# Kernel tuning notes

Hardware: AMD Instinct MI355X
Metric: run time of the kernel (lower is better)

## Reference

```python
import jax, jax.numpy as jnp
import numpy as np

N_IN = 16384
G = 64            # input grid resolution
K_UP = 8          # 2^3 children per voxel for kernel=2 stride=2 generative transpose conv
N_OUT = N_IN * K_UP
G2 = 2 * G        # output grid resolution
NUMS = 32768      # top-k prune budget
C = 64


def _np_coords_and_maps():
    """Build voxel coords, the 27-offset kernel map on upsampled coords, and a fake GT mask."""
    rng = np.random.default_rng(0)
    flat = rng.choice(G ** 3, size=N_IN, replace=False)
    c = np.stack(np.unravel_index(flat, (G, G, G)), axis=1).astype(np.int64)  # [N_IN,3]
    offs2 = np.stack(np.meshgrid(*([[0, 1]] * 3), indexing='ij'), -1).reshape(-1, 3)  # [8,3]
    cu = (2 * c[:, None, :] + offs2[None]).reshape(-1, 3)  # [N_OUT,3], order n*8+k
    lut = np.full(G2 ** 3, N_OUT, dtype=np.int64)
    key = (cu[:, 0] * G2 + cu[:, 1]) * G2 + cu[:, 2]
    lut[key] = np.arange(N_OUT)
    offs3 = np.stack(np.meshgrid(*([[-1, 0, 1]] * 3), indexing='ij'), -1).reshape(-1, 3)  # [27,3]
    nbr = np.empty((27, N_OUT), np.int64)
    for k, d in enumerate(offs3):
        q = cu + d
        valid = ((q >= 0) & (q < G2)).all(1)
        qk = np.where(valid, (q[:, 0] * G2 + q[:, 1]) * G2 + q[:, 2], 0)
        nbr[k] = np.where(valid, lut[qk], N_OUT)  # N_OUT = sentinel 'missing'
    gt = rng.random(N_OUT) < 0.3  # isin(out.C, ground_truth.C) membership mask
    return nbr.astype(np.int32), gt


def setup_inputs() -> dict:
    key = jax.random.key(0)
    ks = jax.random.split(key, 10)
    nbr, gt = _np_coords_and_maps()
    s = 0.05
    rn = lambda k, shape: jax.random.normal(k, shape, jnp.float32) * s
    z = lambda shape: jnp.zeros(shape, jnp.float32)
    return {
        "x_feats": jax.random.normal(ks[0], (N_IN, C), jnp.float32),
        "Wup": rn(ks[1], (K_UP, C, C)), "bup": z((C,)),
        "Wc0": rn(ks[2], (27, C, C)), "bc0": z((C,)),
        "W00": rn(ks[3], (3, 27, C, C // 4)), "b00": z((3, C // 4)),
        "W01": rn(ks[4], (3, 27, C // 4, C // 2)), "b01": z((3, C // 2)),
        "W10": rn(ks[5], (3, C, C // 4)), "b10": z((3, C // 4)),
        "W11": rn(ks[6], (3, 27, C // 4, C // 4)), "b11": z((3, C // 4)),
        "W12": rn(ks[7], (3, C // 4, C // 2)), "b12": z((3, C // 2)),
        "Wcls": rn(ks[8], (27, C, 1)), "bcls": z((1,)),
        "nbr_idx": jnp.asarray(nbr), "mask_true": jnp.asarray(gt),
        "nums": NUMS,
    }


def sparse_conv(feats, nbr, W, b):
    """Gather-GEMM-scatter sparse conv: feats [N,Cin], nbr [K,N] (N = missing), W [K,Cin,Cout]."""
    fp = jnp.concatenate([feats, jnp.zeros((1, feats.shape[1]), feats.dtype)], axis=0)
    def body(acc, wn):
        Wk, nk = wn
        return acc + fp[nk] @ Wk, None
    acc0 = jnp.zeros((feats.shape[0], W.shape[-1]), feats.dtype)
    out, _ = jax.lax.scan(body, acc0, (W, nbr))
    return out + b


def reference(x_feats, Wup, bup, Wc0, bc0, W00, b00, W01, b01, W10, b10, W11, b11, W12, b12, Wcls, bcls, nbr_idx, mask_true, nums):
    # generative transpose conv k=2 s=2: each voxel emits 8 children (no overlaps)
    up = jnp.einsum('nc,kcd->nkd', x_feats, Wup).reshape(-1, Wup.shape[-1]) + bup  # [N_OUT,C]
    out = jax.nn.relu(up)
    out = jax.nn.relu(sparse_conv(out, nbr_idx, Wc0, bc0))
    for i in range(3):  # 3 InceptionResNet blocks
        o0 = sparse_conv(jax.nn.relu(sparse_conv(out, nbr_idx, W00[i], b00[i])), nbr_idx, W01[i], b01[i])
        t = jax.nn.relu(out @ W10[i] + b10[i])            # 1x1 conv
        t = jax.nn.relu(sparse_conv(t, nbr_idx, W11[i], b11[i]))
        o1 = t @ W12[i] + b12[i]                          # 1x1 conv
        out = jnp.concatenate([o0, o1], axis=1) + out
    out_cls = sparse_conv(out, nbr_idx, Wcls, bcls)       # [N_OUT,1]
    _, idx = jax.lax.top_k(out_cls[:, 0], nums)           # istopk
    mask = jnp.zeros((out.shape[0],), bool).at[idx].set(True) | mask_true  # topk + isin(GT)
    pruned = out * mask[:, None].astype(out.dtype)        # pruning as mask (static shape)
    return out_cls, pruned, mask
```

## Files before the change

kernel.cpp:

```cpp
#include <hip/hip_runtime.h>
#include <cstdint>

#define NOUTC 131072
#define NINC  16384
#define CAP   204800
#define NCH   128
#define MAXB  3328

using uint = unsigned int;

__device__ __forceinline__ uint fkey(float v){
  uint u = __float_as_uint(v);
  return (u & 0x80000000u) ? ~u : (u | 0x80000000u);
}

__device__ __forceinline__ int ktap(int o, int q){
  int d0 = ((q>>2)&1) - ((o>>2)&1);
  int d1 = ((q>>1)&1) - ((o>>1)&1);
  int d2 = (q&1) - (o&1);
  return (d0+1)*9 + (d1+1)*3 + (d2+1);
}
__device__ __forceinline__ bool is_sib(int o, int k){
  int k0 = k/9, k1 = (k%9)/3, k2 = k%3;
  int q0 = ((o>>2)&1) + k0 - 1;
  int q1 = ((o>>1)&1) + k1 - 1;
  int q2 = (o&1)      + k2 - 1;
  return (q0>=0 && q0<=1 && q1>=0 && q1<=1 && q2>=0 && q2<=1);
}

__global__ __launch_bounds__(256)
void count_kernel(const int* __restrict__ nbr, uint* __restrict__ counts)
{
  int k = blockIdx.x / NCH, cb = blockIdx.x % NCH;
  int t = threadIdx.x;
  int cnt = 0;
  for (int s = 0; s < 4; ++s){
    int row = cb*1024 + s*256 + t;
    int idx = nbr[(size_t)k*NOUTC + row];
    bool f = (idx != NOUTC) && !is_sib(row & 7, k);
    cnt += __syncthreads_count(f);
  }
  if (t == 0) counts[blockIdx.x] = (uint)cnt;
}

__global__ __launch_bounds__(256)
void scan_kernel(const uint* __restrict__ counts, uint* __restrict__ choff,
                 int* __restrict__ karr)
{
  __shared__ uint kt[27], segs[27], sege[27];
  int t = threadIdx.x;
  if (t < 27){ uint s = 0; for (int cb = 0; cb < NCH; ++cb) s += counts[t*NCH+cb]; kt[t] = s; }
  __syncthreads();
  if (t == 0){
    uint run = 0;
    for (int k = 0; k < 27; ++k){
      segs[k] = run;
      uint pad = (kt[k] + 63u) & ~63u;
      if (run + pad > CAP) pad = (run < CAP) ? ((CAP - run) & ~63u) : 0;
      run += pad;
      sege[k] = run;
    }
  }
  __syncthreads();
  if (t < 27){
    uint run = segs[t];
    for (int cb = 0; cb < NCH; ++cb){ choff[t*NCH+cb] = run; run += counts[t*NCH+cb]; }
  }
  __syncthreads();
  for (int b = t; b < MAXB; b += 256){
    int kk = -1; uint e = (uint)b * 64u;
    for (int k = 0; k < 27; ++k) if (e >= segs[k] && e < sege[k]) kk = k;
    karr[b] = kk;
  }
}

__global__ __launch_bounds__(256)
void fill_kernel(const int* __restrict__ nbr, const uint* __restrict__ choff,
                 uint2* __restrict__ entries)
{
  __shared__ uint wc[4][4];
  __shared__ uint sbase[4];
  int k = blockIdx.x / NCH, cb = blockIdx.x % NCH;
  int t = threadIdx.x, w = t >> 6, l = t & 63;
  uint base = choff[blockIdx.x];
  int rows[4], idxs[4];
  unsigned long long bal[4];
  for (int s = 0; s < 4; ++s){
    int row = cb*1024 + s*256 + t;
    int idx = nbr[(size_t)k*NOUTC + row];
    bool f = (idx != NOUTC) && !is_sib(row & 7, k);
    bal[s] = __ballot(f);
    if (l == 0) wc[s][w] = (uint)__popcll(bal[s]);
    rows[s] = row; idxs[s] = idx;
  }
  __syncthreads();
  if (t == 0){
    uint r = 0;
    for (int s = 0; s < 4; ++s){ sbase[s] = r; for (int w2 = 0; w2 < 4; ++w2) r += wc[s][w2]; }
  }
  __syncthreads();
  for (int s = 0; s < 4; ++s){
    if ((bal[s] >> l) & 1ull){
      uint off = sbase[s];
      for (int w2 = 0; w2 < w; ++w2) off += wc[s][w2];
      off += (uint)__popcll(bal[s] & ((1ull << l) - 1ull));
      uint pos = base + off;
      if (pos < CAP) entries[pos] = make_uint2((uint)rows[s], (uint)idxs[s]);
    }
  }
}

__global__ __launch_bounds__(256)
void c0sib_kernel(const float* __restrict__ feats, const float* __restrict__ Wc0,
                  const float* __restrict__ bias, float* __restrict__ outp)
{
  __shared__ float smem[1280 + 14688];
  float* ft = smem;
  float* wb = smem + 1280;
  const int t = threadIdx.x, w = t >> 6, l = t & 63;
  const int o = l >> 3, pg = (l >> 2) & 1, cg = l & 3;
  const int base = blockIdx.x * 128;

  int kt8[8];
  #pragma unroll
  for (int q = 0; q < 8; ++q) kt8[q] = ktap(o, q);

  float acc[8][16];
  #pragma unroll
  for (int a = 0; a < 8; ++a)
    #pragma unroll
    for (int j = 0; j < 16; ++j) acc[a][j] = 0.f;

  for (int ch = 0; ch < 8; ++ch){
    {
      int row = base + (t >> 1), part = t & 1;
      float4 v = *reinterpret_cast<const float4*>(feats + (size_t)row*64 + ch*8 + part*4);
      int oo = row & 7, pp = (row >> 3) & 15;
      int cl = part * 4;
      ft[((cl+0)*8 + oo)*20 + pp] = v.x;
      ft[((cl+1)*8 + oo)*20 + pp] = v.y;
      ft[((cl+2)*8 + oo)*20 + pp] = v.z;
      ft[((cl+3)*8 + oo)*20 + pp] = v.w;
    }
    for (int e = t; e < 3456; e += 256){
      int c4 = e & 15, kk = (e >> 4) % 27, ci = (e >> 4) / 27;
      float4 v = *reinterpret_cast<const float4*>(Wc0 + (size_t)kk*4096 + (ch*8+ci)*64 + c4*4);
      *reinterpret_cast<float4*>(&wb[(ci*27 + kk)*68 + c4*4]) = v;
    }
    __syncthreads();
    #pragma unroll
    for (int ii = 0; ii < 2; ++ii){
      int ci = w * 2 + ii;
      #pragma unroll
      for (int q = 0; q < 8; ++q){
        const float* fp = &ft[(ci*8 + q)*20 + pg*8];
        float4 f0 = *reinterpret_cast<const float4*>(fp);
        float4 f1 = *reinterpret_cast<const float4*>(fp + 4);
        float fv[8] = {f0.x,f0.y,f0.z,f0.w, f1.x,f1.y,f1.z,f1.w};
        const float* wp = &wb[(ci*27 + kt8[q])*68 + cg*16];
        float4 w0 = *reinterpret_cast<const float4*>(wp);
        float4 w1 = *reinterpret_cast<const float4*>(wp + 4);
        float4 w2 = *reinterpret_cast<const float4*>(wp + 8);
        float4 w3 = *reinterpret_cast<const float4*>(wp + 12);
        float wv[16] = {w0.x,w0.y,w0.z,w0.w, w1.x,w1.y,w1.z,w1.w,
                        w2.x,w2.y,w2.z,w2.w, w3.x,w3.y,w3.z,w3.w};
        #pragma unroll
        for (int a = 0; a < 8; ++a)
          #pragma unroll
          for (int j = 0; j < 16; ++j)
            acc[a][j] = fmaf(fv[a], wv[j], acc[a][j]);
      }
    }
    __syncthreads();
  }

  float* red = wb;
  #pragma unroll
  for (int hh = 0; hh < 2; ++hh){
    if (w >= 2){
      float* d = &red[((w-2)*64 + l)*68];
      #pragma unroll
      for (int a = 0; a < 8; ++a){
        float4 v0 = {acc[a][hh*8+0], acc[a][hh*8+1], acc[a][hh*8+2], acc[a][hh*8+3]};
        float4 v1 = {acc[a][hh*8+4], acc[a][hh*8+5], acc[a][hh*8+6], acc[a][hh*8+7]};
        *reinterpret_cast<float4*>(d + a*8)     = v0;
        *reinterpret_cast<float4*>(d + a*8 + 4) = v1;
      }
    }
    __syncthreads();
    if (w < 2){
      const float* s2 = &red[(w*64 + l)*68];
      #pragma unroll
      for (int a = 0; a < 8; ++a)
        #pragma unroll
        for (int j = 0; j < 8; ++j) acc[a][hh*8+j] += s2[a*8+j];
    }
    __syncthreads();
    if (w == 1){
      float* d = &red[l*68];
      #pragma unroll
      for (int a = 0; a < 8; ++a)
        #pragma unroll
        for (int j = 0; j < 8; ++j) d[a*8+j] = acc[a][hh*8+j];
    }
    __syncthreads();
    if (w == 0){
      const float* s2 = &red[l*68];
      #pragma unroll
      for (int a = 0; a < 8; ++a)
        #pragma unroll
        for (int j = 0; j < 8; ++j) acc[a][hh*8+j] += s2[a*8+j];
    }
    __syncthreads();
  }

  if (w == 0){
    #pragma unroll
    for (int pp = 0; pp < 8; ++pp){
      int row = base + (pg*8 + pp)*8 + o;
      float* dst = outp + (size_t)row*64 + cg*16;
      #pragma unroll
      for (int m = 0; m < 4; ++m){
        float4 v = {acc[pp][m*4+0] + bias[cg*16+m*4+0],
                    acc[pp][m*4+1] + bias[cg*16+m*4+1],
                    acc[pp][m*4+2] + bias[cg*16+m*4+2],
                    acc[pp][m*4+3] + bias[cg*16+m*4+3]};
        *reinterpret_cast<float4*>(dst + m*4) = v;
      }
    }
  }
}

__global__ __launch_bounds__(256)
void asib_kernel(const float* __restrict__ feats, const float* __restrict__ W00i,
                 const float* __restrict__ b00i, float* __restrict__ t0)
{
  __shared__ float smem[8704];
  float* ft = smem;
  float* wb = smem + 2304;
  const int t = threadIdx.x, w = t >> 6, l = t & 63;
  const int o = l >> 3, pg = l & 7;
  const int base = blockIdx.x * 256;

  int kt8[8];
  #pragma unroll
  for (int q = 0; q < 8; ++q) kt8[q] = ktap(o, q);

  float acc[4][16];
  #pragma unroll
  for (int a = 0; a < 4; ++a)
    #pragma unroll
    for (int j = 0; j < 16; ++j) acc[a][j] = 0.f;

  for (int ch = 0; ch < 8; ++ch){
    {
      int row = base + t;
      float4 v0 = *reinterpret_cast<const float4*>(feats + (size_t)row*64 + ch*8);
      float4 v1 = *reinterpret_cast<const float4*>(feats + (size_t)row*64 + ch*8 + 4);
      int oo = row & 7, pp = (row >> 3) & 31;
      ft[((0)*8 + oo)*36 + pp] = v0.x; ft[((1)*8 + oo)*36 + pp] = v0.y;
      ft[((2)*8 + oo)*36 + pp] = v0.z; ft[((3)*8 + oo)*36 + pp] = v0.w;
      ft[((4)*8 + oo)*36 + pp] = v1.x; ft[((5)*8 + oo)*36 + pp] = v1.y;
      ft[((6)*8 + oo)*36 + pp] = v1.z; ft[((7)*8 + oo)*36 + pp] = v1.w;
    }
    for (int e = t; e < 864; e += 256){
      int c4 = e & 3, kk = (e >> 2) % 27, ci = (e >> 2) / 27;
      float4 v = *reinterpret_cast<const float4*>(W00i + (size_t)kk*1024 + (ch*8+ci)*16 + c4*4);
      *reinterpret_cast<float4*>(&wb[(ci*27 + kk)*20 + c4*4]) = v;
    }
    __syncthreads();
    #pragma unroll
    for (int ii = 0; ii < 2; ++ii){
      int ci = w * 2 + ii;
      #pragma unroll
      for (int q = 0; q < 8; ++q){
        float4 f0 = *reinterpret_cast<const float4*>(&ft[(ci*8 + q)*36 + pg*4]);
        float fv[4] = {f0.x, f0.y, f0.z, f0.w};
        const float* wp = &wb[(ci*27 + kt8[q])*20];
        float4 w0 = *reinterpret_cast<const float4*>(wp);
        float4 w1 = *reinterpret_cast<const float4*>(wp + 4);
        float4 w2 = *reinterpret_cast<const float4*>(wp + 8);
        float4 w3 = *reinterpret_cast<const float4*>(wp + 12);
        float wv[16] = {w0.x,w0.y,w0.z,w0.w, w1.x,w1.y,w1.z,w1.w,
                        w2.x,w2.y,w2.z,w2.w, w3.x,w3.y,w3.z,w3.w};
        #pragma unroll
        for (int a = 0; a < 4; ++a)
          #pragma unroll
          for (int j = 0; j < 16; ++j)
            acc[a][j] = fmaf(fv[a], wv[j], acc[a][j]);
      }
    }
    __syncthreads();
  }

  float* red = smem;
  if (w >= 2){
    float* d = &red[((w-2)*64 + l)*68];
    #pragma unroll
    for (int a = 0; a < 4; ++a){
      #pragma unroll
      for (int m = 0; m < 4; ++m){
        float4 v = {acc[a][m*4+0], acc[a][m*4+1], acc[a][m*4+2], acc[a][m*4+3]};
        *reinterpret_cast<float4*>(d + a*16 + m*4) = v;
      }
    }
  }
  __syncthreads();
  if (w < 2){
    const float* s2 = &red[(w*64 + l)*68];
    #pragma unroll
    for (int a = 0; a < 4; ++a)
      #pragma unroll
      for (int j = 0; j < 16; ++j) acc[a][j] += s2[a*16+j];
  }
  __syncthreads();
  if (w == 1){
    float* d = &red[l*68];
    #pragma unroll
    for (int a = 0; a < 4; ++a)
      #pragma unroll
      for (int j = 0; j < 16; ++j) d[a*16+j] = acc[a][j];
  }
  __syncthreads();
  if (w == 0){
    const float* s2 = &red[l*68];
    #pragma unroll
    for (int a = 0; a < 4; ++a)
      #pragma unroll
      for (int j = 0; j < 16; ++j) acc[a][j] += s2[a*16+j];
    #pragma unroll
    for (int pp = 0; pp < 4; ++pp){
      int row = base + (pg*4 + pp)*8 + o;
      float* dst = t0 + (size_t)row*16;
      #pragma unroll
      for (int m = 0; m < 4; ++m){
        float4 v = {acc[pp][m*4+0] + b00i[m*4+0], acc[pp][m*4+1] + b00i[m*4+1],
                    acc[pp][m*4+2] + b00i[m*4+2], acc[pp][m*4+3] + b00i[m*4+3]};
        *reinterpret_cast<float4*>(dst + m*4) = v;
      }
    }
  }
}

__global__ __launch_bounds__(128)
void p1c0_kernel(const float* __restrict__ feats, const float* __restrict__ Wc0,
                 const uint2* __restrict__ entries, const int* __restrict__ karr,
                 float* __restrict__ slab, int h)
{
  __shared__ float ft2[64*68];
  __shared__ float wbs[64*36];
  int b = blockIdx.x;
  int k = karr[b];
  if (k < 0) return;
  int t = threadIdx.x;
  for (int e = t; e < 512; e += 128){
    int ci = e >> 3, c4 = e & 7;
    float4 v = *reinterpret_cast<const float4*>(Wc0 + (size_t)k*4096 + ci*64 + h*32 + c4*4);
    *reinterpret_cast<float4*>(&wbs[ci*36 + c4*4]) = v;
  }
  {
    int e = t >> 1, part = t & 1;
    uint2 en = entries[(size_t)b*64 + e];
    int gidx = (en.x == 0xFFFFFFFFu) ? NOUTC : (int)en.y;
    const float4* src = reinterpret_cast<const float4*>(feats + (size_t)gidx*64 + part*32);
    #pragma unroll
    for (int j = 0; j < 8; ++j){
      float4 v = src[j];
      int ci = part*32 + j*4;
      ft2[(ci+0)*68 + e] = v.x; ft2[(ci+1)*68 + e] = v.y;
      ft2[(ci+2)*68 + e] = v.z; ft2[(ci+3)*68 + e] = v.w;
    }
  }
  __syncthreads();
  int sp = t & 1, tile = t >> 1, eg = tile >> 3, cg = tile & 7;
  float acc[8][4];
  #pragma unroll
  for (int a = 0; a < 8; ++a){ acc[a][0]=0.f; acc[a][1]=0.f; acc[a][2]=0.f; acc[a][3]=0.f; }
  for (int i = 0; i < 32; ++i){
    int ci = sp + 2*i;
    float4 f0 = *reinterpret_cast<const float4*>(&ft2[ci*68 + eg*8]);
    float4 f1 = *reinterpret_cast<const float4*>(&ft2[ci*68 + eg*8 + 4]);
    float fv[8] = {f0.x,f0.y,f0.z,f0.w, f1.x,f1.y,f1.z,f1.w};
    float4 wv = *reinterpret_cast<const float4*>(&wbs[ci*36 + cg*4]);
    float wa[4] = {wv.x, wv.y, wv.z, wv.w};
    #pragma unroll
    for (int a = 0; a < 8; ++a)
      #pragma unroll
      for (int j = 0; j < 4; ++j)
        acc[a][j] = fmaf(fv[a], wa[j], acc[a][j]);
  }
  #pragma unroll
  for (int a = 0; a < 8; ++a)
    #pragma unroll
    for (int j = 0; j < 4; ++j) acc[a][j] += __shfl_xor(acc[a][j], 1, 64);
  if (sp == 0){
    #pragma unroll
    for (int a = 0; a < 8; ++a){
      int e = eg*8 + a;
      float4 v = {acc[a][0], acc[a][1], acc[a][2], acc[a][3]};
      *reinterpret_cast<float4*>(&slab[((size_t)b*64 + e)*32 + cg*4]) = v;
    }
  }
}

__global__ __launch_bounds__(128)
void p1a_kernel(const float* __restrict__ feats, const float* __restrict__ W00i,
                const uint2* __restrict__ entries, const int* __restrict__ karr,
                float* __restrict__ slab)
{
  __shared__ float ft2[64*68];
  __shared__ float wbs[64*18];
  int b = blockIdx.x;
  int k = karr[b];
  if (k < 0) return;
  int t = threadIdx.x;
  for (int e = t; e < 256; e += 128){
    int ci = e >> 2, c4 = e & 3;
    float4 v = *reinterpret_cast<const float4*>(W00i + (size_t)k*1024 + ci*16 + c4*4);
    *reinterpret_cast<float4*>(&wbs[ci*18 + c4*4]) = v;
  }
  {
    int e = t >> 1, part = t & 1;
    uint2 en = entries[(size_t)b*64 + e];
    int gidx = (en.x == 0xFFFFFFFFu) ? NOUTC : (int)en.y;
    const float4* src = reinterpret_cast<const float4*>(feats + (size_t)gidx*64 + part*32);
    #pragma unroll
    for (int j = 0; j < 8; ++j){
      float4 v = src[j];
      int ci = part*32 + j*4;
      ft2[(ci+0)*68 + e] = v.x; ft2[(ci+1)*68 + e] = v.y;
      ft2[(ci+2)*68 + e] = v.z; ft2[(ci+3)*68 + e] = v.w;
    }
  }
  __syncthreads();
  int sp = t & 1, tile = t >> 1, eg = tile >> 2, cg = tile & 3;
  float acc[4][4];
  #pragma unroll
  for (int a = 0; a < 4; ++a){ acc[a][0]=0.f; acc[a][1]=0.f; acc[a][2]=0.f; acc[a][3]=0.f; }
  for (int i = 0; i < 32; ++i){
    int ci = sp + 2*i;
    float4 f0 = *reinterpret_cast<const float4*>(&ft2[ci*68 + eg*4]);
    float fv[4] = {f0.x, f0.y, f0.z, f0.w};
    float4 wv = *reinterpret_cast<const float4*>(&wbs[ci*18 + cg*4]);
    float wa[4] = {wv.x, wv.y, wv.z, wv.w};
    #pragma unroll
    for (int a = 0; a < 4; ++a)
      #pragma unroll
      for (int j = 0; j < 4; ++j)
        acc[a][j] = fmaf(fv[a], wa[j], acc[a][j]);
  }
  #pragma unroll
  for (int a = 0; a < 4; ++a)
    #pragma unroll
    for (int j = 0; j < 4; ++j) acc[a][j] += __shfl_xor(acc[a][j], 1, 64);
  if (sp == 0){
    #pragma unroll
    for (int a = 0; a < 4; ++a){
      int e = eg*4 + a;
      float4 v = {acc[a][0], acc[a][1], acc[a][2], acc[a][3]};
      *reinterpret_cast<float4*>(&slab[((size_t)b*64 + e)*16 + cg*4]) = v;
    }
  }
}

__global__ __launch_bounds__(256)
void cmbc0_kernel(const int* __restrict__ nbr, const uint* __restrict__ choff,
                  const float* __restrict__ slab, float* __restrict__ fb, int h)
{
  __shared__ uint wc[4][4];
  int cb = blockIdx.x >> 1, cq = blockIdx.x & 1;
  int t = threadIdx.x, w = t >> 6, l = t & 63;
  int co0 = h*32 + cq*16;
  float acc[4][16];
  #pragma unroll
  for (int s = 0; s < 4; ++s)
    #pragma unroll
    for (int j = 0; j < 16; ++j) acc[s][j] = 0.f;

  for (int k = 0; k < 27; ++k){
    unsigned long long bal[4];
    for (int s = 0; s < 4; ++s){
      int row = cb*1024 + s*256 + t;
      int idx = nbr[(size_t)k*NOUTC + row];
      bool f = (idx != NOUTC) && !is_sib(row & 7, k);
      bal[s] = __ballot(f);
      if (l == 0) wc[s][w] = (uint)__popcll(bal[s]);
    }
    __syncthreads();
    uint sbs[4];
    { uint r = 0; for (int s = 0; s < 4; ++s){ sbs[s] = r; for (int w2 = 0; w2 < 4; ++w2) r += wc[s][w2]; } }
    uint base = choff[k*NCH + cb];
    for (int s = 0; s < 4; ++s){
      if ((bal[s] >> l) & 1ull){
        uint off = sbs[s];
        for (int w2 = 0; w2 < w; ++w2) off += wc[s][w2];
        off += (uint)__popcll(bal[s] & ((1ull << l) - 1ull));
        uint pos = base + off;
        if (pos < CAP){
          const float4* sr = reinterpret_cast<const float4*>(slab + (size_t)pos*32 + cq*16);
          float4 a0 = sr[0], a1 = sr[1], a2 = sr[2], a3 = sr[3];
          acc[s][0]+=a0.x; acc[s][1]+=a0.y; acc[s][2]+=a0.z; acc[s][3]+=a0.w;
          acc[s][4]+=a1.x; acc[s][5]+=a1.y; acc[s][6]+=a1.z; acc[s][7]+=a1.w;
          acc[s][8]+=a2.x; acc[s][9]+=a2.y; acc[s][10]+=a2.z; acc[s][11]+=a2.w;
          acc[s][12]+=a3.x; acc[s][13]+=a3.y; acc[s][14]+=a3.z; acc[s][15]+=a3.w;
        }
      }
    }
    __syncthreads();
  }
  for (int s = 0; s < 4; ++s){
    int row = cb*1024 + s*256 + t;
    float* dst = fb + (size_t)row*64 + co0;
    #pragma unroll
    for (int m = 0; m < 4; ++m){
      float4 b0 = *reinterpret_cast<const float4*>(dst + m*4);
      float4 v;
      v.x = b0.x + acc[s][m*4+0]; v.x = v.x > 0.f ? v.x : 0.f;
      v.y = b0.y + acc[s][m*4+1]; v.y = v.y > 0.f ? v.y : 0.f;
      v.z = b0.z + acc[s][m*4+2]; v.z = v.z > 0.f ? v.z : 0.f;
      v.w = b0.w + acc[s][m*4+3]; v.w = v.w > 0.f ? v.w : 0.f;
      *reinterpret_cast<float4*>(dst + m*4) = v;
    }
  }
}

__global__ __launch_bounds__(256)
void cmba_kernel(const int* __restrict__ nbr, const uint* __restrict__ choff,
                 const float* __restrict__ slab, float* __restrict__ t0)
{
  __shared__ uint wc[4][4];
  int cb = blockIdx.x;
  int t = threadIdx.x, w = t >> 6, l = t & 63;
  float acc[4][16];
  #pragma unroll
  for (int s = 0; s < 4; ++s)
    #pragma unroll
    for (int j = 0; j < 16; ++j) acc[s][j] = 0.f;

  for (int k = 0; k < 27; ++k){
    unsigned long long bal[4];
    for (int s = 0; s < 4; ++s){
      int row = cb*1024 + s*256 + t;
      int idx = nbr[(size_t)k*NOUTC + row];
      bool f = (idx != NOUTC) && !is_sib(row & 7, k);
      bal[s] = __ballot(f);
      if (l == 0) wc[s][w] = (uint)__popcll(bal[s]);
    }
    __syncthreads();
    uint sbs[4];
    { uint r = 0; for (int s = 0; s < 4; ++s){ sbs[s] = r; for (int w2 = 0; w2 < 4; ++w2) r += wc[s][w2]; } }
    uint base = choff[k*NCH + cb];
    for (int s = 0; s < 4; ++s){
      if ((bal[s] >> l) & 1ull){
        uint off = sbs[s];
        for (int w2 = 0; w2 < w; ++w2) off += wc[s][w2];
        off += (uint)__popcll(bal[s] & ((1ull << l) - 1ull));
        uint pos = base + off;
        if (pos < CAP){
          const float4* sr = reinterpret_cast<const float4*>(slab + (size_t)pos*16);
          float4 a0 = sr[0], a1 = sr[1], a2 = sr[2], a3 = sr[3];
          acc[s][0]+=a0.x; acc[s][1]+=a0.y; acc[s][2]+=a0.z; acc[s][3]+=a0.w;
          acc[s][4]+=a1.x; acc[s][5]+=a1.y; acc[s][6]+=a1.z; acc[s][7]+=a1.w;
          acc[s][8]+=a2.x; acc[s][9]+=a2.y; acc[s][10]+=a2.z; acc[s][11]+=a2.w;
          acc[s][12]+=a3.x; acc[s][13]+=a3.y; acc[s][14]+=a3.z; acc[s][15]+=a3.w;
        }
      }
    }
    __syncthreads();
  }
  for (int s = 0; s < 4; ++s){
    int row = cb*1024 + s*256 + t;
    float* dst = t0 + (size_t)row*16;
    #pragma unroll
    for (int m = 0; m < 4; ++m){
      float4 b0 = *reinterpret_cast<const float4*>(dst + m*4);
      float4 v;
      v.x = b0.x + acc[s][m*4+0]; v.x = v.x > 0.f ? v.x : 0.f;
      v.y = b0.y + acc[s][m*4+1]; v.y = v.y > 0.f ? v.y : 0.f;
      v.z = b0.z + acc[s][m*4+2]; v.z = v.z > 0.f ? v.z : 0.f;
      v.w = b0.w + acc[s][m*4+3]; v.w = v.w > 0.f ? v.w : 0.f;
      *reinterpret_cast<float4*>(dst + m*4) = v;
    }
  }
}

template<int ROWS, int CIN, int COUT, int SPLIT, int THREADS, int NK,
         bool IDENT, bool RELU, bool RESID>
__global__ __launch_bounds__(THREADS)
void spconv2(const float* __restrict__ feats, const int* __restrict__ nbr,
             const float* __restrict__ Wg, const float* __restrict__ bias,
             const float* __restrict__ resid, float* __restrict__ outp,
             int ostride, int coff)
{
  constexpr int RG = ROWS / 8, CG = COUT / 8;
  static_assert(RG * CG * SPLIT == THREADS, "bad thread tiling");
  constexpr int CIPT = CIN / SPLIT;
  constexpr int STR  = ROWS + 4;
  constexpr int WSTR = COUT + 4;
  constexpr int TPR  = THREADS / ROWS;
  constexpr int FSTG = CIN / TPR;
  constexpr int WSTG = (CIN * COUT) / THREADS;
  constexpr int NSLOT = THREADS / SPLIT;

  constexpr int MAIN_FL = CIN * STR + CIN * WSTR;
  constexpr int RED_FL  = (SPLIT > 1) ? (THREADS / 2) * 64 : 0;
  constexpr int LDS_FL  = MAIN_FL > RED_FL ? MAIN_FL : RED_FL;
  __shared__ float smem[LDS_FL];
  float* ft = smem;
  float* Wl = smem + CIN * STR;

  const int t    = threadIdx.x;
  const int base = blockIdx.x * ROWS;
  const int sp   = t % SPLIT;
  const int slot = t / SPLIT;
  const int rg = slot / CG, cg = slot % CG;
  const int trr = rg * 8, tcc = cg * 8;
  const int gr = t / TPR, part = t % TPR;

  float4 fstg[FSTG / 4];
  alignas(16) float wstg[WSTG];
  float acc[8][8];
  #pragma unroll
  for (int a = 0; a < 8; ++a)
    #pragma unroll
    for (int b = 0; b < 8; ++b) acc[a][b] = 0.f;

  auto load_f = [&](int k) {
    int gidx = IDENT ? (base + gr) : nbr[(size_t)k * NOUTC + base + gr];
    const float4* src = reinterpret_cast<const float4*>(feats + (size_t)gidx * CIN + part * FSTG);
    #pragma unroll
    for (int j = 0; j < FSTG / 4; ++j) fstg[j] = src[j];
  };
  auto load_w = [&](int k) {
    const float* wsrc = Wg + (size_t)k * CIN * COUT + t * WSTG;
    if constexpr (WSTG % 4 == 0) {
      #pragma unroll
      for (int m = 0; m < WSTG / 4; ++m)
        *reinterpret_cast<float4*>(&wstg[4 * m]) = reinterpret_cast<const float4*>(wsrc)[m];
    } else {
      *reinterpret_cast<float2*>(&wstg[0]) = *reinterpret_cast<const float2*>(wsrc);
    }
  };
// ... 64 lines not shown

  if (sp == 0) {
    #pragma unroll
    for (int a = 0; a < 8; ++a) {
      int r = base + trr + a;
      float o[8];
      #pragma unroll
      for (int b = 0; b < 8; ++b) {
        float v = acc[a][b] + bias[tcc + b];
        if (RELU) v = v > 0.f ? v : 0.f;
        o[b] = v;
      }
      if (RESID) {
        const float* rs = resid + (size_t)r * 64 + coff + tcc;
        float4 r0 = *reinterpret_cast<const float4*>(rs);
        float4 r1 = *reinterpret_cast<const float4*>(rs + 4);
        o[0] += r0.x; o[1] += r0.y; o[2] += r0.z; o[3] += r0.w;
        o[4] += r1.x; o[5] += r1.y; o[6] += r1.z; o[7] += r1.w;
      }
      float* dst = outp + (size_t)r * ostride + coff + tcc;
      float4 s0 = {o[0], o[1], o[2], o[3]};
      float4 s1 = {o[4], o[5], o[6], o[7]};
      *reinterpret_cast<float4*>(dst)     = s0;
      *reinterpret_cast<float4*>(dst + 4) = s1;
    }
  }
}

__global__ __launch_bounds__(256)
void upsample_kernel(const float* __restrict__ x, const float* __restrict__ Wup,
                     const float* __restrict__ bup, float* __restrict__ outp)
{
  __shared__ float Wl[64 * 64];
  __shared__ float xt[64][68];
  const int t    = threadIdx.x;
  const int tile = blockIdx.x >> 3;
  const int k    = blockIdx.x & 7;
  const int base = tile * 64;

  #pragma unroll
  for (int i = t; i < 4096; i += 256) Wl[i] = Wup[k * 4096 + i];
  {
    const int gr = t >> 2, gp = t & 3;
    const float4* src = reinterpret_cast<const float4*>(x + (size_t)(base + gr) * 64) + gp * 4;
    #pragma unroll
    for (int j = 0; j < 4; ++j) {
      float4 v = src[j];
      int ci = (gp * 4 + j) * 4;
      xt[ci + 0][gr] = v.x; xt[ci + 1][gr] = v.y;
      xt[ci + 2][gr] = v.z; xt[ci + 3][gr] = v.w;
    }
  }
  __syncthreads();
  const int tcc = (t % 16) * 4, trr = (t / 16) * 4;
  float acc[4][4];
  #pragma unroll
  for (int a = 0; a < 4; ++a)
    #pragma unroll
    for (int b = 0; b < 4; ++b) acc[a][b] = 0.f;
  #pragma unroll
  for (int ci = 0; ci < 64; ++ci) {
    float4 f = *reinterpret_cast<const float4*>(&xt[ci][trr]);
    float4 w = *reinterpret_cast<const float4*>(&Wl[ci * 64 + tcc]);
    float fv[4] = {f.x, f.y, f.z, f.w};
    float wv[4] = {w.x, w.y, w.z, w.w};
    #pragma unroll
    for (int a = 0; a < 4; ++a)
      #pragma unroll
      for (int b = 0; b < 4; ++b) acc[a][b] = fmaf(fv[a], wv[b], acc[a][b]);
  }
  #pragma unroll
  for (int a = 0; a < 4; ++a) {
    int n = base + trr + a;
    float4 o;
    float v0 = acc[a][0] + bup[tcc + 0]; o.x = v0 > 0.f ? v0 : 0.f;
    float v1 = acc[a][1] + bup[tcc + 1]; o.y = v1 > 0.f ? v1 : 0.f;
    float v2 = acc[a][2] + bup[tcc + 2]; o.z = v2 > 0.f ? v2 : 0.f;
    float v3 = acc[a][3] + bup[tcc + 3]; o.w = v3 > 0.f ? v3 : 0.f;
    *reinterpret_cast<float4*>(outp + ((size_t)n * 8 + k) * 64 + tcc) = o;
  }
}

__global__ __launch_bounds__(256)
void cls1_kernel(const float* __restrict__ feats, const float* __restrict__ Wcls,
                 float* __restrict__ g)
{
  const int n = blockIdx.x * 256 + threadIdx.x;
  if (blockIdx.x == 0 && threadIdx.x < 28) g[(size_t)NOUTC * 28 + threadIdx.x] = 0.f;
  const float4* src = reinterpret_cast<const float4*>(feats + (size_t)n * 64);
  float f[64];
  #pragma unroll
  for (int j = 0; j < 16; ++j) {
    float4 a = src[j];
    f[4*j+0]=a.x; f[4*j+1]=a.y; f[4*j+2]=a.z; f[4*j+3]=a.w;
  }
  #pragma unroll 1
  for (int k = 0; k < 27; ++k) {
    const float* w = Wcls + k * 64;
    float s0 = 0.f, s1 = 0.f, s2 = 0.f, s3 = 0.f;
    #pragma unroll
    for (int j = 0; j < 16; ++j) {
      s0 = fmaf(f[j],      w[j],      s0);
      s1 = fmaf(f[16 + j], w[16 + j], s1);
      s2 = fmaf(f[32 + j], w[32 + j], s2);
      s3 = fmaf(f[48 + j], w[48 + j], s3);
    }
    g[(size_t)n * 28 + k] = (s0 + s1) + (s2 + s3);
  }
}

__global__ __launch_bounds__(256)
void cls2_kernel(const float* __restrict__ g, const int* __restrict__ nbr,
                 const float* __restrict__ bcls, float* __restrict__ out_cls)
{
  const int n = blockIdx.x * 256 + threadIdx.x;
  float s = bcls[0];
  #pragma unroll 1
  for (int k = 0; k < 27; ++k) {
    int idx = nbr[(size_t)k * NOUTC + n];
    s += g[(size_t)idx * 28 + k];
  }
  out_cls[n] = s;
}

__global__ void init_kernel(uint* hist1, uint* hist2, int* tie_cnt, int* flag,
                            float* fa, float* fb, float* t0, float* t1)
{
  int i = blockIdx.x * 256 + threadIdx.x;
  if (i < 65536) hist1[i] = 0;
  else if (i < 131072) hist2[i - 65536] = 0;
  if (i == 0) { tie_cnt[0] = 0; flag[0] = 0; }
  if (i < 64) { fa[(size_t)NOUTC * 64 + i] = 0.f; fb[(size_t)NOUTC * 64 + i] = 0.f; }
  if (i < 16) { t0[(size_t)NOUTC * 16 + i] = 0.f; t1[(size_t)NOUTC * 16 + i] = 0.f; }
}

__global__ void detect_kernel(const unsigned char* __restrict__ mt, int* flag)
{
  int i = blockIdx.x * 256 + threadIdx.x;
  int p = i * 4 + 1;
  if (p < NOUTC && mt[p] != 0) flag[0] = 1;
}

__global__ void hist1_kernel(const float* __restrict__ cls, uint* __restrict__ hist)
{
  for (int i = blockIdx.x * blockDim.x + threadIdx.x; i < NOUTC; i += gridDim.x * blockDim.x)
    atomicAdd(&hist[fkey(cls[i]) >> 16], 1u);
}

__global__ void scan1_kernel(const uint* __restrict__ hist, const int* __restrict__ nums,
                             uint* __restrict__ res)
{
  __shared__ uint chunk[256];
  const int t = threadIdx.x;
  uint s = 0;
  for (int j = 0; j < 256; ++j) s += hist[t * 256 + j];
  chunk[t] = s;
  __syncthreads();
  if (t == 0) {
    uint k = (uint)nums[0];
    uint cum = 0; int c = 255;
    for (; c > 0; --c) { if (cum + chunk[c] >= k) break; cum += chunk[c]; }
    int B = c * 256; uint cum2 = cum;
    for (int b = c * 256 + 255; b >= c * 256; --b) {
      if (cum2 + hist[b] >= k) { B = b; break; }
      cum2 += hist[b];
    }
    res[0] = (uint)B; res[1] = cum2;
  }
}

__global__ void hist2_kernel(const float* __restrict__ cls, const uint* __restrict__ res1,
                             uint* __restrict__ hist)
{
  const uint B = res1[0];
  for (int i = blockIdx.x * blockDim.x + threadIdx.x; i < NOUTC; i += gridDim.x * blockDim.x) {
    uint key = fkey(cls[i]);
    if ((key >> 16) == B) atomicAdd(&hist[key & 0xffffu], 1u);
  }
}

__global__ void scan2_kernel(const uint* __restrict__ hist, const uint* __restrict__ res1,
                             const int* __restrict__ nums, uint* __restrict__ res2)
{
  __shared__ uint chunk[256];
  const int t = threadIdx.x;
  uint s = 0;
  for (int j = 0; j < 256; ++j) s += hist[t * 256 + j];
  chunk[t] = s;
  __syncthreads();
  if (t == 0) {
    uint k = (uint)nums[0];
    uint cum = res1[1]; int c = 255;
    for (; c > 0; --c) { if (cum + chunk[c] >= k) break; cum += chunk[c]; }
    int L = c * 256; uint cum2 = cum;
    for (int b = c * 256 + 255; b >= c * 256; --b) {
      if (cum2 + hist[b] >= k) { L = b; break; }
      cum2 += hist[b];
    }
    res2[0] = (res1[0] << 16) | (uint)L;
    res2[1] = k - cum2;
  }
}

__global__ void mark_kernel(const float* __restrict__ cls, const uint* __restrict__ res2,
                            unsigned char* __restrict__ msel, int* tie_cnt, int* tie_idx)
{
  const uint T = res2[0];
  for (int i = blockIdx.x * blockDim.x + threadIdx.x; i < NOUTC; i += gridDim.x * blockDim.x) {
    uint key = fkey(cls[i]);
    msel[i] = key > T ? 1 : 0;
    if (key == T) {
      int p = atomicAdd(tie_cnt, 1);
      if (p < 4096) tie_idx[p] = i;
    }
  }
}

__global__ void tie_kernel(const uint* __restrict__ res2, const int* __restrict__ tie_cnt,
                           const int* __restrict__ tie_idx, unsigned char* __restrict__ msel)
{
  int need = (int)res2[1];
  int cnt = tie_cnt[0]; if (cnt > 4096) cnt = 4096;
  if (need <= 0) return;
  if (cnt <= need) {
    for (int i = threadIdx.x; i < cnt; i += 256) msel[tie_idx[i]] = 1;
  } else {
    for (int i = threadIdx.x; i < cnt; i += 256) {
      int my = tie_idx[i];
      int rank = 0;
      for (int j = 0; j < cnt; ++j) rank += (tie_idx[j] < my) ? 1 : 0;
      if (rank < need) msel[my] = 1;
    }
  }
}

__global__ void prune_kernel(const float* __restrict__ feats, const unsigned char* __restrict__ msel,
                             const void* __restrict__ mtrue, const int* __restrict__ flag,
                             float* __restrict__ dout)
{
  const unsigned char* mb = (const unsigned char*)mtrue;
  const int* mi = (const int*)mtrue;
  const bool bytes = (flag[0] != 0);
  float* pruned = dout + NOUTC;
  float* maskf  = dout + NOUTC + (size_t)NOUTC * 64;
  const float4* src = reinterpret_cast<const float4*>(feats);
  float4* dst = reinterpret_cast<float4*>(pruned);
  const int total = NOUTC * 16;
  for (int i = blockIdx.x * blockDim.x + threadIdx.x; i < total; i += gridDim.x * blockDim.x) {
    int n = i >> 4;
    bool mt = bytes ? (mb[n] != 0) : (mi[n] != 0);
    bool m = (msel[n] != 0) || mt;
    float4 v = src[i];
    float4 z = {0.f, 0.f, 0.f, 0.f};
    dst[i] = m ? v : z;
    if ((i & 15) == 0) maskf[n] = m ? 1.f : 0.f;
  }
}

extern "C" void kernel_launch(void* const* d_in, const int* in_sizes, int n_in,
                              void* d_out, int out_size, void* d_ws, size_t ws_size,
                              hipStream_t stream)
{
  const float* x    = (const float*)d_in[0];
  const float* Wup  = (const float*)d_in[1];
  const float* bup  = (const float*)d_in[2];
  const float* Wc0  = (const float*)d_in[3];
  const float* bc0  = (const float*)d_in[4];
  const float* W00  = (const float*)d_in[5];
  const float* b00  = (const float*)d_in[6];
  const float* W01  = (const float*)d_in[7];
  const float* b01  = (const float*)d_in[8];
  const float* W10  = (const float*)d_in[9];
  const float* b10  = (const float*)d_in[10];
  const float* W11  = (const float*)d_in[11];
  const float* b11  = (const float*)d_in[12];
  const float* W12  = (const float*)d_in[13];
  const float* b12  = (const float*)d_in[14];
  const float* Wcls = (const float*)d_in[15];
  const float* bcls = (const float*)d_in[16];
  const int*   nbr  = (const int*)d_in[17];
  const void*  mtrue= d_in[18];
  const int*   nums = (const int*)d_in[19];

  float* dout = (float*)d_out;

  float* fa   = (float*)d_ws;
  float* t0   = fa + (size_t)(NOUTC + 1) * 64;
  float* t1   = t0 + (size_t)(NOUTC + 1) * 16;
  float* g    = t0;
  float* slab = t1 + (size_t)(NOUTC + 1) * 16;
  uint*  hist1 = (uint*)(slab + (size_t)CAP * 32);
  uint*  hist2 = hist1 + 65536;
  uint*  res1  = hist2 + 65536;
  uint*  res2  = res1 + 2;
  int*   tie_cnt = (int*)(res2 + 2);
  int*   flag    = tie_cnt + 1;
  int*   tie_idx = flag + 1;
  uint*  counts  = (uint*)(tie_idx + 4096);
  uint*  choff   = counts + 27 * NCH;
  int*   karr    = (int*)(choff + 27 * NCH);
  int*   meta    = karr + MAXB;
  uint2* entries = (uint2*)(meta + 4);
  unsigned char* msel = (unsigned char*)(entries + CAP);
  float* fb = dout + NOUTC;

  init_kernel<<<512, 256, 0, stream>>>(hist1, hist2, tie_cnt, flag, fa, fb, t0, t1);
  detect_kernel<<<128, 256, 0, stream>>>((const unsigned char*)mtrue, flag);

  hipMemsetAsync(entries, 0xFF, (size_t)CAP * sizeof(uint2), stream);
  count_kernel<<<27 * NCH, 256, 0, stream>>>(nbr, counts);
  scan_kernel<<<1, 256, 0, stream>>>(counts, choff, karr);
  fill_kernel<<<27 * NCH, 256, 0, stream>>>(nbr, choff, entries);

  upsample_kernel<<<2048, 256, 0, stream>>>(x, Wup, bup, fa);

  c0sib_kernel<<<1024, 256, 0, stream>>>(fa, Wc0, bc0, fb);
  p1c0_kernel<<<MAXB, 128, 0, stream>>>(fa, Wc0, entries, karr, slab, 0);
  cmbc0_kernel<<<256, 256, 0, stream>>>(nbr, choff, slab, fb, 0);
  p1c0_kernel<<<MAXB, 128, 0, stream>>>(fa, Wc0, entries, karr, slab, 1);
  cmbc0_kernel<<<256, 256, 0, stream>>>(nbr, choff, slab, fb, 1);

  const float* cur = fb; float* nxt = fa;
  for (int i = 0; i < 3; ++i) {
    const float* W00i = W00 + (size_t)i * 27 * 1024;
    asib_kernel<<<512, 256, 0, stream>>>(cur, W00i, b00 + i * 16, t0);
    p1a_kernel<<<MAXB, 128, 0, stream>>>(cur, W00i, entries, karr, slab);
    cmba_kernel<<<128, 256, 0, stream>>>(nbr, choff, slab, t0);
    spconv2<128, 64, 16, 4, 128, 1, true, true, false>
        <<<NOUTC / 128, 128, 0, stream>>>(cur, nullptr, W10 + (size_t)i * 1024,
                                          b10 + i * 16, nullptr, t1, 16, 0);
    spconv2<128, 16, 32, 4, 256, 27, false, false, true>
        <<<NOUTC / 128, 256, 0, stream>>>(t0, nbr, W01 + (size_t)i * 27 * 512,
                                          b01 + i * 32, cur, nxt, 64, 0);
    spconv2<128, 16, 16, 4, 128, 27, false, true, false>
        <<<NOUTC / 128, 128, 0, stream>>>(t1, nbr, W11 + (size_t)i * 27 * 256,
                                          b11 + i * 16, nullptr, t0, 16, 0);
    spconv2<128, 16, 32, 4, 256, 1, true, false, true>
        <<<NOUTC / 128, 256, 0, stream>>>(t0, nullptr, W12 + (size_t)i * 512,
                                          b12 + i * 32, cur, nxt, 64, 32);
    float* tmp = (float*)cur; cur = nxt; nxt = tmp;
  }

  cls1_kernel<<<512, 256, 0, stream>>>(cur, Wcls, g);
  cls2_kernel<<<512, 256, 0, stream>>>(g, nbr, bcls, dout);

  hist1_kernel<<<512, 256, 0, stream>>>(dout, hist1);
  scan1_kernel<<<1, 256, 0, stream>>>(hist1, nums, res1);
  hist2_kernel<<<512, 256, 0, stream>>>(dout, res1, hist2);
  scan2_kernel<<<1, 256, 0, stream>>>(hist2, res1, nums, res2);
  mark_kernel<<<512, 256, 0, stream>>>(dout, res2, msel, tie_cnt, tie_idx);
  tie_kernel<<<1, 256, 0, stream>>>(res2, tie_cnt, tie_idx, msel);
  prune_kernel<<<4096, 256, 0, stream>>>(cur, msel, mtrue, flag, dout);
}
```

Before: 1.445 ms.

## Recast sibling-tap convolutions as dense GEMMs over per-parent 8-voxel groups

Replaces the custom c0sib and asib kernels, which gathered the sibling taps within each 8-child group, with a generic register-tiled SGEMM. Each parent's 8 children are treated as one 512-wide row, multiplied by a prebuilt block weight matrix that maps every (input sibling, output sibling) pair to its kernel tap. Small prep kernels build these expanded weight matrices each call. The aim is a regular, well-pipelined GEMM with double-buffered global loads in place of the tap-indexed smem layout and the cross-wave reduction. In exchange it adds extra weight-prep launches and more weight traffic.

```diff
diff --git a/kernel.cpp b/kernel.cpp
--- a/kernel.cpp
+++ b/kernel.cpp
@@ -26,6 +26,133 @@
   int q1 = ((o>>1)&1) + k1 - 1;
   int q2 = (o&1)      + k2 - 1;
   return (q0>=0 && q0<=1 && q1>=0 && q1<=1 && q2>=0 && q2<=1);
+}
+
+__global__ __launch_bounds__(256)
+void ww_prep_c0(const float* __restrict__ Wc0, float* __restrict__ WW)
+{
+  int tid = blockIdx.x * 256 + threadIdx.x;
+  int col = tid & 511, rowk = tid >> 9;
+  int o = col >> 6, co = col & 63;
+  int q = rowk >> 6, ci = rowk & 63;
+  WW[tid] = Wc0[ktap(o, q) * 4096 + ci * 64 + co];
+}
+
+__global__ __launch_bounds__(256)
+void ww_prep_a(const float* __restrict__ W00i, float* __restrict__ WW2)
+{
+  int tid = blockIdx.x * 256 + threadIdx.x;
+  int col = tid & 127, rowk = tid >> 7;
+  int o = col >> 4, co = col & 15;
+  int q = rowk >> 6, ci = rowk & 63;
+  WW2[tid] = W00i[ktap(o, q) * 1024 + ci * 16 + co];
+}
+
+template<int BLKM, int TM, int BMASK>
+__global__ __launch_bounds__(256)
+void gemm_ww(const float* __restrict__ A, const float* __restrict__ Bw,
+             const float* __restrict__ bias, float* __restrict__ C, int N)
+{
+  constexpr int MGR  = BLKM / TM;
+  constexpr int NGR  = 256 / MGR;
+  constexpr int BLKN = NGR * 8;
+  static_assert(MGR * NGR == 256, "bad tiling");
+  constexpr int ASTR = BLKM + 4;
+  constexpr int BSTR = BLKN + 4;
+  constexpr int ALD  = BLKM / 32;
+  constexpr int BLD  = BLKN / 32;
+  __shared__ float As[32 * ASTR];
+  __shared__ float Bs[32 * BSTR];
+
+  const int t  = threadIdx.x;
+  const int MBC = 16384 / BLKM;
+  const int mb = blockIdx.x % MBC;
+  const int nb = blockIdx.x / MBC;
+  const int mg = t / NGR, ng = t % NGR;
+
+  float4 ast[ALD], bst[BLD];
+  float acc[TM][8];
+  #pragma unroll
+  for (int a = 0; a < TM; ++a)
+    #pragma unroll
+    for (int b = 0; b < 8; ++b) acc[a][b] = 0.f;
+
+  auto load_a = [&](int kc){
+    #pragma unroll
+    for (int i2 = 0; i2 < ALD; ++i2){
+      int idx = t + i2 * 256;
+      int row = idx >> 3, c4 = idx & 7;
+      ast[i2] = *reinterpret_cast<const float4*>(
+          A + (size_t)(mb * BLKM + row) * 512 + kc * 32 + c4 * 4);
+    }
+  };
+  auto load_b = [&](int kc){
+    #pragma unroll
+    for (int i2 = 0; i2 < BLD; ++i2){
+      int idx = t + i2 * 256;
+      int kk = idx >> 5, c4 = idx & 31;
+      bst[i2] = *reinterpret_cast<const float4*>(
+          Bw + (size_t)(kc * 32 + kk) * N + nb * BLKN + c4 * 4);
+    }
+  };
+
+  load_a(0); load_b(0);
+
+  for (int kc = 0; kc < 16; ++kc){
+    #pragma unroll
+    for (int i2 = 0; i2 < ALD; ++i2){
+      int idx = t + i2 * 256;
+      int row = idx >> 3, c4 = idx & 7;
+      As[(c4*4+0)*ASTR + row] = ast[i2].x;
+      As[(c4*4+1)*ASTR + row] = ast[i2].y;
+      As[(c4*4+2)*ASTR + row] = ast[i2].z;
+      As[(c4*4+3)*ASTR + row] = ast[i2].w;
+    }
+    #pragma unroll
+    for (int i2 = 0; i2 < BLD; ++i2){
+      int idx = t + i2 * 256;
+      int kk = idx >> 5, c4 = idx & 31;
+      *reinterpret_cast<float4*>(&Bs[kk * BSTR + c4 * 4]) = bst[i2];
+    }
+    __syncthreads();
+    if (kc < 15){ load_a(kc + 1); load_b(kc + 1); }
+    #pragma unroll 4
+    for (int kk = 0; kk < 32; ++kk){
+      float av[TM];
+      if constexpr (TM == 8){
+        float4 a0 = *reinterpret_cast<const float4*>(&As[kk*ASTR + mg*8]);
+        float4 a1 = *reinterpret_cast<const float4*>(&As[kk*ASTR + mg*8 + 4]);
+        av[0]=a0.x; av[1]=a0.y; av[2]=a0.z; av[3]=a0.w;
+        av[4]=a1.x; av[5]=a1.y; av[6]=a1.z; av[7]=a1.w;
+      } else {
+        float4 a0 = *reinterpret_cast<const float4*>(&As[kk*ASTR + mg*4]);
+        av[0]=a0.x; av[1]=a0.y; av[2]=a0.z; av[3]=a0.w;
+      }
+      float4 b0 = *reinterpret_cast<const float4*>(&Bs[kk*BSTR + ng*8]);
+      float4 b1 = *reinterpret_cast<const float4*>(&Bs[kk*BSTR + ng*8 + 4]);
+      float bv[8] = {b0.x,b0.y,b0.z,b0.w, b1.x,b1.y,b1.z,b1.w};
+      #pragma unroll
+      for (int a = 0; a < TM; ++a)
+        #pragma unroll
+        for (int b = 0; b < 8; ++b)
+          acc[a][b] = fmaf(av[a], bv[b], acc[a][b]);
+    }
+    __syncthreads();
+  }
+
+  const int colbase = nb * BLKN + ng * 8;
+  float bvals[8];
+  #pragma unroll
+  for (int b = 0; b < 8; ++b) bvals[b] = bias[(colbase + b) & BMASK];
+  #pragma unroll
+  for (int a = 0; a < TM; ++a){
+    int row = mb * BLKM + mg * TM + a;
+    float* dst = C + (size_t)row * N + colbase;
+    float4 o0 = {acc[a][0]+bvals[0], acc[a][1]+bvals[1], acc[a][2]+bvals[2], acc[a][3]+bvals[3]};
+    float4 o1 = {acc[a][4]+bvals[4], acc[a][5]+bvals[5], acc[a][6]+bvals[6], acc[a][7]+bvals[7]};
+    *reinterpret_cast<float4*>(dst)     = o0;
+    *reinterpret_cast<float4*>(dst + 4) = o1;
+  }
 }
 
 __global__ __launch_bounds__(256)
@@ -106,238 +233,6 @@
       off += (uint)__popcll(bal[s] & ((1ull << l) - 1ull));
       uint pos = base + off;
       if (pos < CAP) entries[pos] = make_uint2((uint)rows[s], (uint)idxs[s]);
-    }
-  }
-}
-
-__global__ __launch_bounds__(256)
-void c0sib_kernel(const float* __restrict__ feats, const float* __restrict__ Wc0,
-                  const float* __restrict__ bias, float* __restrict__ outp)
-{
-  __shared__ float smem[1280 + 14688];
-  float* ft = smem;
-  float* wb = smem + 1280;
-  const int t = threadIdx.x, w = t >> 6, l = t & 63;
-  const int o = l >> 3, pg = (l >> 2) & 1, cg = l & 3;
-  const int base = blockIdx.x * 128;
-
-  int kt8[8];
-  #pragma unroll
-  for (int q = 0; q < 8; ++q) kt8[q] = ktap(o, q);
-
-  float acc[8][16];
-  #pragma unroll
-  for (int a = 0; a < 8; ++a)
-    #pragma unroll
-    for (int j = 0; j < 16; ++j) acc[a][j] = 0.f;
-
-  for (int ch = 0; ch < 8; ++ch){
-    {
-      int row = base + (t >> 1), part = t & 1;
-      float4 v = *reinterpret_cast<const float4*>(feats + (size_t)row*64 + ch*8 + part*4);
-      int oo = row & 7, pp = (row >> 3) & 15;
-      int cl = part * 4;
-      ft[((cl+0)*8 + oo)*20 + pp] = v.x;
-      ft[((cl+1)*8 + oo)*20 + pp] = v.y;
-      ft[((cl+2)*8 + oo)*20 + pp] = v.z;
-      ft[((cl+3)*8 + oo)*20 + pp] = v.w;
-    }
-    for (int e = t; e < 3456; e += 256){
-      int c4 = e & 15, kk = (e >> 4) % 27, ci = (e >> 4) / 27;
-      float4 v = *reinterpret_cast<const float4*>(Wc0 + (size_t)kk*4096 + (ch*8+ci)*64 + c4*4);
-      *reinterpret_cast<float4*>(&wb[(ci*27 + kk)*68 + c4*4]) = v;
-    }
-    __syncthreads();
-    #pragma unroll
-    for (int ii = 0; ii < 2; ++ii){
-      int ci = w * 2 + ii;
-      #pragma unroll
-      for (int q = 0; q < 8; ++q){
-        const float* fp = &ft[(ci*8 + q)*20 + pg*8];
-        float4 f0 = *reinterpret_cast<const float4*>(fp);
-        float4 f1 = *reinterpret_cast<const float4*>(fp + 4);
-        float fv[8] = {f0.x,f0.y,f0.z,f0.w, f1.x,f1.y,f1.z,f1.w};
-        const float* wp = &wb[(ci*27 + kt8[q])*68 + cg*16];
-        float4 w0 = *reinterpret_cast<const float4*>(wp);
-        float4 w1 = *reinterpret_cast<const float4*>(wp + 4);
-        float4 w2 = *reinterpret_cast<const float4*>(wp + 8);
-        float4 w3 = *reinterpret_cast<const float4*>(wp + 12);
-        float wv[16] = {w0.x,w0.y,w0.z,w0.w, w1.x,w1.y,w1.z,w1.w,
-                        w2.x,w2.y,w2.z,w2.w, w3.x,w3.y,w3.z,w3.w};
-        #pragma unroll
-        for (int a = 0; a < 8; ++a)
-          #pragma unroll
-          for (int j = 0; j < 16; ++j)
-            acc[a][j] = fmaf(fv[a], wv[j], acc[a][j]);
-      }
-    }
-    __syncthreads();
-  }
-
-  float* red = wb;
-  #pragma unroll
-  for (int hh = 0; hh < 2; ++hh){
-    if (w >= 2){
-      float* d = &red[((w-2)*64 + l)*68];
-      #pragma unroll
-      for (int a = 0; a < 8; ++a){
-        float4 v0 = {acc[a][hh*8+0], acc[a][hh*8+1], acc[a][hh*8+2], acc[a][hh*8+3]};
-        float4 v1 = {acc[a][hh*8+4], acc[a][hh*8+5], acc[a][hh*8+6], acc[a][hh*8+7]};
-        *reinterpret_cast<float4*>(d + a*8)     = v0;
-        *reinterpret_cast<float4*>(d + a*8 + 4) = v1;
-      }
-    }
-    __syncthreads();
-    if (w < 2){
-      const float* s2 = &red[(w*64 + l)*68];
-      #pragma unroll
-      for (int a = 0; a < 8; ++a)
-        #pragma unroll
-        for (int j = 0; j < 8; ++j) acc[a][hh*8+j] += s2[a*8+j];
-    }
-    __syncthreads();
-    if (w == 1){
-      float* d = &red[l*68];
-      #pragma unroll
-      for (int a = 0; a < 8; ++a)
-        #pragma unroll
-        for (int j = 0; j < 8; ++j) d[a*8+j] = acc[a][hh*8+j];
-    }
-    __syncthreads();
-    if (w == 0){
-      const float* s2 = &red[l*68];
-      #pragma unroll
-      for (int a = 0; a < 8; ++a)
-        #pragma unroll
-        for (int j = 0; j < 8; ++j) acc[a][hh*8+j] += s2[a*8+j];
-    }
-    __syncthreads();
-  }
-
-  if (w == 0){
-    #pragma unroll
-    for (int pp = 0; pp < 8; ++pp){
-      int row = base + (pg*8 + pp)*8 + o;
-      float* dst = outp + (size_t)row*64 + cg*16;
-      #pragma unroll
-      for (int m = 0; m < 4; ++m){
-        float4 v = {acc[pp][m*4+0] + bias[cg*16+m*4+0],
-                    acc[pp][m*4+1] + bias[cg*16+m*4+1],
-                    acc[pp][m*4+2] + bias[cg*16+m*4+2],
-                    acc[pp][m*4+3] + bias[cg*16+m*4+3]};
-        *reinterpret_cast<float4*>(dst + m*4) = v;
-      }
-    }
-  }
-}
-
-__global__ __launch_bounds__(256)
-void asib_kernel(const float* __restrict__ feats, const float* __restrict__ W00i,
-                 const float* __restrict__ b00i, float* __restrict__ t0)
-{
-  __shared__ float smem[8704];
-  float* ft = smem;
-  float* wb = smem + 2304;
-  const int t = threadIdx.x, w = t >> 6, l = t & 63;
-  const int o = l >> 3, pg = l & 7;
-  const int base = blockIdx.x * 256;
-
-  int kt8[8];
-  #pragma unroll
-  for (int q = 0; q < 8; ++q) kt8[q] = ktap(o, q);
-
-  float acc[4][16];
-  #pragma unroll
-  for (int a = 0; a < 4; ++a)
-    #pragma unroll
-    for (int j = 0; j < 16; ++j) acc[a][j] = 0.f;
-
-  for (int ch = 0; ch < 8; ++ch){
-    {
-      int row = base + t;
-      float4 v0 = *reinterpret_cast<const float4*>(feats + (size_t)row*64 + ch*8);
-      float4 v1 = *reinterpret_cast<const float4*>(feats + (size_t)row*64 + ch*8 + 4);
-      int oo = row & 7, pp = (row >> 3) & 31;
-      ft[((0)*8 + oo)*36 + pp] = v0.x; ft[((1)*8 + oo)*36 + pp] = v0.y;
-      ft[((2)*8 + oo)*36 + pp] = v0.z; ft[((3)*8 + oo)*36 + pp] = v0.w;
-      ft[((4)*8 + oo)*36 + pp] = v1.x; ft[((5)*8 + oo)*36 + pp] = v1.y;
-      ft[((6)*8 + oo)*36 + pp] = v1.z; ft[((7)*8 + oo)*36 + pp] = v1.w;
-    }
-    for (int e = t; e < 864; e += 256){
-      int c4 = e & 3, kk = (e >> 2) % 27, ci = (e >> 2) / 27;
-      float4 v = *reinterpret_cast<const float4*>(W00i + (size_t)kk*1024 + (ch*8+ci)*16 + c4*4);
-      *reinterpret_cast<float4*>(&wb[(ci*27 + kk)*20 + c4*4]) = v;
-    }
-    __syncthreads();
-    #pragma unroll
-    for (int ii = 0; ii < 2; ++ii){
-      int ci = w * 2 + ii;
-      #pragma unroll
-      for (int q = 0; q < 8; ++q){
-        float4 f0 = *reinterpret_cast<const float4*>(&ft[(ci*8 + q)*36 + pg*4]);
-        float fv[4] = {f0.x, f0.y, f0.z, f0.w};
-        const float* wp = &wb[(ci*27 + kt8[q])*20];
-        float4 w0 = *reinterpret_cast<const float4*>(wp);
-        float4 w1 = *reinterpret_cast<const float4*>(wp + 4);
-        float4 w2 = *reinterpret_cast<const float4*>(wp + 8);
-        float4 w3 = *reinterpret_cast<const float4*>(wp + 12);
-        float wv[16] = {w0.x,w0.y,w0.z,w0.w, w1.x,w1.y,w1.z,w1.w,
-                        w2.x,w2.y,w2.z,w2.w, w3.x,w3.y,w3.z,w3.w};
-        #pragma unroll
-        for (int a = 0; a < 4; ++a)
-          #pragma unroll
-          for (int j = 0; j < 16; ++j)
-            acc[a][j] = fmaf(fv[a], wv[j], acc[a][j]);
-      }
-    }
-    __syncthreads();
-  }
-
-  float* red = smem;
-  if (w >= 2){
-    float* d = &red[((w-2)*64 + l)*68];
-    #pragma unroll
-    for (int a = 0; a < 4; ++a){
-      #pragma unroll
-      for (int m = 0; m < 4; ++m){
-        float4 v = {acc[a][m*4+0], acc[a][m*4+1], acc[a][m*4+2], acc[a][m*4+3]};
-        *reinterpret_cast<float4*>(d + a*16 + m*4) = v;
-      }
-    }
-  }
-  __syncthreads();
-  if (w < 2){
-    const float* s2 = &red[(w*64 + l)*68];
-    #pragma unroll
-    for (int a = 0; a < 4; ++a)
-      #pragma unroll
-      for (int j = 0; j < 16; ++j) acc[a][j] += s2[a*16+j];
-  }
-  __syncthreads();
-  if (w == 1){
-    float* d = &red[l*68];
-    #pragma unroll
-    for (int a = 0; a < 4; ++a)
-      #pragma unroll
-      for (int j = 0; j < 16; ++j) d[a*16+j] = acc[a][j];
-  }
-  __syncthreads();
-  if (w == 0){
-    const float* s2 = &red[l*68];
-    #pragma unroll
-    for (int a = 0; a < 4; ++a)
-      #pragma unroll
-      for (int j = 0; j < 16; ++j) acc[a][j] += s2[a*16+j];
-    #pragma unroll
-    for (int pp = 0; pp < 4; ++pp){
-      int row = base + (pg*4 + pp)*8 + o;
-      float* dst = t0 + (size_t)row*16;
-      #pragma unroll
-      for (int m = 0; m < 4; ++m){
-        float4 v = {acc[pp][m*4+0] + b00i[m*4+0], acc[pp][m*4+1] + b00i[m*4+1],
-                    acc[pp][m*4+2] + b00i[m*4+2], acc[pp][m*4+3] + b00i[m*4+3]};
-        *reinterpret_cast<float4*>(dst + m*4) = v;
-      }
     }
   }
 }
@@ -1008,6 +903,8 @@
   int*   meta    = karr + MAXB;
   uint2* entries = (uint2*)(meta + 4);
   unsigned char* msel = (unsigned char*)(entries + CAP);
+  float* WW   = (float*)(msel + NOUTC);
+  float* WW2  = WW + 262144;
   float* fb = dout + NOUTC;
 
   init_kernel<<<512, 256, 0, stream>>>(hist1, hist2, tie_cnt, flag, fa, fb, t0, t1);
@@ -1017,10 +914,13 @@
   count_kernel<<<27 * NCH, 256, 0, stream>>>(nbr, counts);
   scan_kernel<<<1, 256, 0, stream>>>(counts, choff, karr);
   fill_kernel<<<27 * NCH, 256, 0, stream>>>(nbr, choff, entries);
+  ww_prep_c0<<<1024, 256, 0, stream>>>(Wc0, WW);
+  for (int i = 0; i < 3; ++i)
+    ww_prep_a<<<256, 256, 0, stream>>>(W00 + (size_t)i * 27 * 1024, WW2 + (size_t)i * 65536);
 
   upsample_kernel<<<2048, 256, 0, stream>>>(x, Wup, bup, fa);
 
-  c0sib_kernel<<<1024, 256, 0, stream>>>(fa, Wc0, bc0, fb);
+  gemm_ww<128, 8, 63><<<512, 256, 0, stream>>>(fa, WW, bc0, fb, 512);
   p1c0_kernel<<<MAXB, 128, 0, stream>>>(fa, Wc0, entries, karr, slab, 0);
   cmbc0_kernel<<<256, 256, 0, stream>>>(nbr, choff, slab, fb, 0);
   p1c0_kernel<<<MAXB, 128, 0, stream>>>(fa, Wc0, entries, karr, slab, 1);
@@ -1029,7 +929,8 @@
   const float* cur = fb; float* nxt = fa;
   for (int i = 0; i < 3; ++i) {
     const float* W00i = W00 + (size_t)i * 27 * 1024;
-    asib_kernel<<<512, 256, 0, stream>>>(cur, W00i, b00 + i * 16, t0);
+    gemm_ww<64, 4, 15><<<256, 256, 0, stream>>>(cur, WW2 + (size_t)i * 65536,
+                                                b00 + i * 16, t0, 128);
     p1a_kernel<<<MAXB, 128, 0, stream>>>(cur, W00i, entries, karr, slab);
     cmba_kernel<<<128, 256, 0, stream>>>(nbr, choff, slab, t0);
     spconv2<128, 64, 16, 4, 128, 1, true, true, false>
```

Result: faster. 1.363 ms (-5.7%).
